# Kernel tuning notes

Hardware: AMD Instinct MI355X
Metric: run time of the kernel (lower is better)

## Reference

```python
import math
import jax, jax.numpy as jnp
import numpy as np

N = 50000          # nodes
E = 800000         # edges
IN_DIM = 128
HID = 128
OUT_DIM = 64
LAYER_NUM = 8      # -> LAYER_NUM - 2 = 6 GCN2Conv layers
NUM_CONVS = LAYER_NUM - 2
ALPHA = 0.1
THETA = 0.5
# PyG GCN2Conv: beta = log(theta / layer + 1); here every conv was built with layer = layer_num + 1
BETA = math.log(THETA / (LAYER_NUM + 1) + 1.0)


def setup_inputs() -> dict:
    key = jax.random.key(0)
    ks = jax.random.split(key, 10)
    x = jax.random.normal(ks[0], (N, IN_DIM), dtype=jnp.float32)
    edge_src = jax.random.randint(ks[1], (E,), 0, N, dtype=jnp.int32)
    edge_dst = jax.random.randint(ks[2], (E,), 0, N, dtype=jnp.int32)
    edge_weight = jax.random.uniform(ks[3], (E,), dtype=jnp.float32)
    s0 = 1.0 / math.sqrt(IN_DIM)
    s1 = 1.0 / math.sqrt(HID)
    W0 = jax.random.uniform(ks[4], (IN_DIM, HID), dtype=jnp.float32, minval=-s0, maxval=s0)
    b0 = jnp.zeros((HID,), dtype=jnp.float32)
    W1 = jax.random.uniform(ks[5], (HID, OUT_DIM), dtype=jnp.float32, minval=-s1, maxval=s1)
    b1 = jnp.zeros((OUT_DIM,), dtype=jnp.float32)
    conv_ws = jax.random.uniform(ks[6], (NUM_CONVS, HID, HID), dtype=jnp.float32, minval=-s1, maxval=s1)
    return {"x": x, "edge_src": edge_src, "edge_dst": edge_dst, "edge_weight": edge_weight,
            "W0": W0, "b0": b0, "W1": W1, "b1": b1, "conv_ws": conv_ws}


def reference(x, edge_src, edge_dst, edge_weight, W0, b0, W1, b1, conv_ws):
    # linear[0] + relu (dropout=0.0 -> identity)
    h = jnp.maximum(x @ W0 + b0, 0.0)          # [N, HID]
    x0 = h
    for i in range(NUM_CONVS):
        # weighted neighbor sum: out[i] = sum_{(j->i)} w_ji * h[j]
        msgs = h[edge_src] * edge_weight[:, None]               # [E, HID]
        agg = jax.ops.segment_sum(msgs, edge_dst, num_segments=N)
        # GCN2Conv (shared_weights=True): z = (1-alpha)*Ah + alpha*x0; out = (1-beta)*z + beta*(z W)
        z = agg * (1.0 - ALPHA) + ALPHA * x0
        h = z * (1.0 - BETA) + BETA * (z @ conv_ws[i])
        h = jnp.maximum(h, 0.0)
    return h @ W1 + b1                          # [N, OUT_DIM]
```

## Files before the change

### kernel.cpp

```cpp
#include <hip/hip_runtime.h>
#include <cstdint>
#include <cstddef>


#define NN 50000
#define EE 800000

constexpr float ALPHA   = 0.1f;
constexpr float BETA_C  = 0.05406722127027574f;

constexpr int NB = (NN + 255) / 256;
constexpr int HB = (EE + 255) / 256;
constexpr int PREP_TOT = 128 * 128 + 6 * 128 * 128 + 64 * 128;
constexpr int PB = (PREP_TOT + 255) / 256;
constexpr int SLICE = NN / 8;
constexpr int NCH = (NN + 31) / 32;

typedef unsigned short u16;
typedef unsigned int   u32;
typedef __attribute__((ext_vector_type(8))) short short8;
typedef __attribute__((ext_vector_type(4))) float f32x4;

__device__ __forceinline__ float bf2f(u16 u) {
    union { float f; u32 i; } c; c.i = ((u32)u) << 16; return c.f;
}
__device__ __forceinline__ u16 f2bf(float f) {
    union { float f; u32 i; } c; c.f = f;
    u32 r = c.i + 0x7fffu + ((c.i >> 16) & 1u);
    return (u16)(r >> 16);
}

__global__ void k_hist_prep(const int* __restrict__ edst, int* __restrict__ deg,
                            const float* __restrict__ W0, const float* __restrict__ cw,
                            const float* __restrict__ W1, u16* __restrict__ w0t,
                            u16* __restrict__ wft, u16* __restrict__ w1t, int E) {
    int b = blockIdx.x;
    if (b < HB) {
        int i = b * 256 + threadIdx.x;
        if (i < E) atomicAdd(&deg[edst[i]], 1);
    } else {
        int i = (b - HB) * 256 + threadIdx.x;
        if (i < 16384) {
            int n = i >> 7, k = i & 127;
            w0t[i] = f2bf(W0[k * 128 + n]);
        } else if (i < 16384 + 6 * 16384) {
            int r = i - 16384;
            int l = r >> 14; int t = r & 16383;
            int n = t >> 7, k = t & 127;
            float v = BETA_C * cw[l * 16384 + k * 128 + n]
                      + ((k == n) ? (1.f - BETA_C) : 0.f);
            wft[r] = f2bf(v);
        } else if (i < PREP_TOT) {
            int r = i - (16384 + 6 * 16384);
            int n = r >> 7, k = r & 127;
            w1t[r] = f2bf(W1[k * 64 + n]);
        }
    }
}

__global__ __launch_bounds__(256) void k_scan_lb(const int* __restrict__ deg,
                                                 int* __restrict__ bsum,
                                                 int* __restrict__ offs,
                                                 int* __restrict__ cur) {
    __shared__ int sh[256];
    __shared__ int sw[4];
    const int c = blockIdx.x, tid = threadIdx.x;
    const int i = c * 256 + tid;
    int v = (i < NN) ? deg[i] : 0;
    sh[tid] = v;
    __syncthreads();
#pragma unroll
    for (int o = 1; o < 256; o <<= 1) {
        int u = (tid >= o) ? sh[tid - o] : 0;
        __syncthreads();
        sh[tid] += u;
        __syncthreads();
    }
    if (tid == 255) atomicExch(&bsum[c], sh[255] + 1);
    int part = 0;
    for (int t = tid; t < c; t += 256) {
        int b;
        do { b = atomicAdd(&bsum[t], 0); } while (b == 0);
        part += b - 1;
    }
#pragma unroll
    for (int o = 32; o > 0; o >>= 1) part += __shfl_down(part, o);
    if ((tid & 63) == 0) sw[tid >> 6] = part;
    __syncthreads();
    const int base = sw[0] + sw[1] + sw[2] + sw[3];
    const int ex = base + sh[tid] - v;
    if (i < NN) {
        offs[i] = ex;
        cur[i]  = ex;
        if (i == NN - 1) offs[NN] = ex + v;
    }
}

__global__ void k_bucket_x(const int* __restrict__ src, const int* __restrict__ dst,
                           const float* __restrict__ w, int* __restrict__ cur,
                           u32* __restrict__ ep, int E) {
    const int slice = blockIdx.x & 7;
    const int i = (blockIdx.x >> 3) * 256 + threadIdx.x;
    if (i >= E) return;
    const int d = dst[i];
    const int lo = slice * SLICE;
    if (d >= lo && d < lo + SLICE) {
        int pos = atomicAdd(&cur[d], 1);
        ep[pos] = ((u32)f2bf(w[i]) << 16) | (u32)src[i];
    }
}

__global__ __launch_bounds__(256) void k_agg_z(const int* __restrict__ offs,
                                               const u32* __restrict__ ep,
                                               const u16* __restrict__ hs,
                                               const u16* __restrict__ x0s,
                                               u16* __restrict__ zs) {
    const int lane = threadIdx.x & 63;
    const int wave = threadIdx.x >> 6;
    const int g  = lane >> 3;
    const int f2 = lane & 7;
    const int s  = blockIdx.y;
    const int n  = blockIdx.x * 32 + wave * 8 + g;
    const int nc = n < NN ? n : NN - 1;
    const uint2* table = (const uint2*)(hs + (size_t)s * NN * 32);

    const int beg = offs[nc], end = offs[nc + 1];
    float a0 = 0.f, a1 = 0.f, a2 = 0.f, a3 = 0.f;
    int e = beg;
    for (; e + 7 < end; e += 8) {
        u32 r[8]; uint2 v[8];
#pragma unroll
        for (int j = 0; j < 8; ++j) r[j] = ep[e + j];
#pragma unroll
        for (int j = 0; j < 8; ++j)
            v[j] = table[(size_t)(r[j] & 0xffffu) * 8 + f2];
#pragma unroll
        for (int j = 0; j < 8; ++j) {
            float w = bf2f((u16)(r[j] >> 16));
            a0 += w * bf2f((u16)v[j].x);  a1 += w * bf2f((u16)(v[j].x >> 16));
            a2 += w * bf2f((u16)v[j].y);  a3 += w * bf2f((u16)(v[j].y >> 16));
        }
    }
    for (; e < end; ++e) {
        u32 r = ep[e];
        uint2 v = table[(size_t)(r & 0xffffu) * 8 + f2];
        float w = bf2f((u16)(r >> 16));
        a0 += w * bf2f((u16)v.x);  a1 += w * bf2f((u16)(v.x >> 16));
        a2 += w * bf2f((u16)v.y);  a3 += w * bf2f((u16)(v.y >> 16));
    }
    if (n < NN) {
        const size_t idx = (size_t)s * NN * 8 + (size_t)n * 8 + f2;
        uint2 xv = ((const uint2*)x0s)[idx];
        float z0 = (1.f - ALPHA) * a0 + ALPHA * bf2f((u16)xv.x);
        float z1 = (1.f - ALPHA) * a1 + ALPHA * bf2f((u16)(xv.x >> 16));
        float z2 = (1.f - ALPHA) * a2 + ALPHA * bf2f((u16)xv.y);
        float z3 = (1.f - ALPHA) * a3 + ALPHA * bf2f((u16)(xv.y >> 16));
        uint2 o;
        o.x = (u32)f2bf(z0) | ((u32)f2bf(z1) << 16);
        o.y = (u32)f2bf(z2) | ((u32)f2bf(z3) << 16);
        ((uint2*)zs)[idx] = o;
    }
}

template <int MODE>
__global__ __launch_bounds__(256) void k_gemm_mfma(const void* __restrict__ Av,
                                                   const u16* __restrict__ Wt,
                                                   const float* __restrict__ bias,
                                                   void* __restrict__ Cv, int M) {
    constexpr int NT = (MODE == 2) ? 4 : 8;
    const int lane = threadIdx.x & 63;
    const int wave = threadIdx.x >> 6;
    const int q = lane >> 4;
    const int m16 = lane & 15;
    const int node = blockIdx.x * 64 + wave * 16 + m16;
    const int nload = node < M ? node : M - 1;

    short8 zf[4];
    if (MODE == 0) {
        const float* xp = (const float*)Av + (size_t)nload * 128 + q * 8;
#pragma unroll
        for (int s = 0; s < 4; ++s) {
            float4 u0 = *(const float4*)(xp + s * 32);
            float4 u1 = *(const float4*)(xp + s * 32 + 4);
            short8 z;
            z[0] = (short)f2bf(u0.x); z[1] = (short)f2bf(u0.y);
            z[2] = (short)f2bf(u0.z); z[3] = (short)f2bf(u0.w);
            z[4] = (short)f2bf(u1.x); z[5] = (short)f2bf(u1.y);
            z[6] = (short)f2bf(u1.z); z[7] = (short)f2bf(u1.w);
            zf[s] = z;
        }
    } else {
        const u16* ap = (const u16*)Av;
#pragma unroll
        for (int s = 0; s < 4; ++s)
            zf[s] = *(const short8*)(ap + (size_t)s * NN * 32 + (size_t)nload * 32 + q * 8);
    }

    f32x4 acc[NT];
#pragma unroll
    for (int c = 0; c < NT; ++c) {
        f32x4 a = {0.f, 0.f, 0.f, 0.f};
        const u16* wp = Wt + (size_t)(c * 16 + m16) * 128 + q * 8;
#pragma unroll
        for (int s = 0; s < 4; ++s) {
            short8 wf = *(const short8*)(wp + s * 32);
            a = __builtin_amdgcn_mfma_f32_16x16x32_bf16(wf, zf[s], a, 0, 0, 0);
        }
        acc[c] = a;
    }

    if (node < M) {
#pragma unroll
        for (int c = 0; c < NT; ++c) {
            const int f0 = c * 16 + q * 4;
            if (MODE == 2) {
                float4 bv = *(const float4*)(bias + f0);
                float4 o;
                o.x = acc[c][0] + bv.x; o.y = acc[c][1] + bv.y;
                o.z = acc[c][2] + bv.z; o.w = acc[c][3] + bv.w;
                *(float4*)((float*)Cv + (size_t)node * 64 + f0) = o;
            } else {
                float v0 = acc[c][0], v1 = acc[c][1], v2 = acc[c][2], v3 = acc[c][3];
                if (MODE == 0) {
                    float4 bv = *(const float4*)(bias + f0);
                    v0 += bv.x; v1 += bv.y; v2 += bv.z; v3 += bv.w;
                }
                v0 = v0 > 0.f ? v0 : 0.f;
                v1 = v1 > 0.f ? v1 : 0.f;
                v2 = v2 > 0.f ? v2 : 0.f;
                v3 = v3 > 0.f ? v3 : 0.f;
                ushort4 o;
                o.x = f2bf(v0); o.y = f2bf(v1); o.z = f2bf(v2); o.w = f2bf(v3);
                *(ushort4*)((u16*)Cv + (size_t)(f0 >> 5) * NN * 32
                            + (size_t)node * 32 + (f0 & 31)) = o;
            }
        }
    }
}


extern "C" void kernel_launch(void* const* d_in, const int* in_sizes, int n_in,
                              void* d_out, int out_size, void* d_ws, size_t ws_size,
                              hipStream_t stream) {
    const float* x    = (const float*)d_in[0];
    const int*   esrc = (const int*)d_in[1];
    const int*   edst = (const int*)d_in[2];
    const float* ew   = (const float*)d_in[3];
    const float* W0   = (const float*)d_in[4];
    const float* b0   = (const float*)d_in[5];
    const float* W1   = (const float*)d_in[6];
    const float* b1   = (const float*)d_in[7];
    const float* cw   = (const float*)d_in[8];
    float* out = (float*)d_out;

    const int N = NN, E = EE;

    u32*  ep4   = (u32*)d_ws;
    u16*  x0s   = (u16*)(ep4 + E);
    u16*  hb1   = x0s + (size_t)4 * N * 32;
    u16*  hb2   = hb1 + (size_t)4 * N * 32;
    u16*  zsb   = hb2 + (size_t)4 * N * 32;
    u16*  w0t   = zsb + (size_t)4 * N * 32;
    u16*  wft   = w0t + 128 * 128;
    u16*  w1t   = wft + 6 * 128 * 128;
    int*  deg   = (int*)(w1t + 64 * 128);
    int*  bsum  = deg  + N;
    int*  offs  = bsum + NB;
    int*  cur   = offs + N + 1;

    hipMemsetAsync(deg, 0, (size_t)(N + NB) * sizeof(int), stream);
    k_hist_prep<<<HB + PB, 256, 0, stream>>>(edst, deg, W0, cw, W1, w0t, wft, w1t, E);
    k_scan_lb<<<NB, 256, 0, stream>>>(deg, bsum, offs, cur);
    k_bucket_x<<<HB * 8, 256, 0, stream>>>(esrc, edst, ew, cur, ep4, E);

    const int gx = (N + 63) / 64;
    const dim3 ga(NCH, 4);

    k_gemm_mfma<0><<<gx, 256, 0, stream>>>(x, w0t, b0, x0s, N);

    const u16* hin = x0s;
    u16* houts[6] = {hb1, hb2, hb1, hb2, hb1, hb2};
    for (int i = 0; i < 6; ++i) {
        k_agg_z<<<ga, 256, 0, stream>>>(offs, ep4, hin, x0s, zsb);
        k_gemm_mfma<1><<<gx, 256, 0, stream>>>(zsb, wft + (size_t)i * 16384,
                                               nullptr, houts[i], N);
        hin = houts[i];
    }

    k_gemm_mfma<2><<<gx, 256, 0, stream>>>(hb2, w1t, b1, out, N);
}
```

Measured before the change: 552.4 us.

## Widen aggregation gathers to 16B per lane and fuse last conv with output GEMM

The aggregation kernel now gives each lane 8 features with uint4 gathers, so 4 lanes cover a 32-feature slice and 16 nodes fit per wave instead of 8. This halves the number of gather instructions and doubles the nodes handled per block. The final conv GEMM and the output projection are fused into one kernel that stages the relu'd hidden tile in LDS, which removes one launch and one hidden-state round trip through global memory. The cost is higher register use in aggregation, fewer lanes per node to spread per-node work, and an extra LDS pass plus a barrier.

After: 546.0 us. About the same (-1.1%).

```diff
diff --git a/kernel.cpp b/kernel.cpp
--- a/kernel.cpp
+++ b/kernel.cpp
@@ -14,7 +14,7 @@
 constexpr int PREP_TOT = 128 * 128 + 6 * 128 * 128 + 64 * 128;
 constexpr int PB = (PREP_TOT + 255) / 256;
 constexpr int SLICE = NN / 8;
-constexpr int NCH = (NN + 31) / 32;
+constexpr int GA = (NN + 63) / 64;
 
 typedef unsigned short u16;
 typedef unsigned int   u32;
@@ -117,48 +117,59 @@
                                                u16* __restrict__ zs) {
     const int lane = threadIdx.x & 63;
     const int wave = threadIdx.x >> 6;
-    const int g  = lane >> 3;
-    const int f2 = lane & 7;
+    const int g  = lane >> 2;
+    const int f4 = lane & 3;
     const int s  = blockIdx.y;
-    const int n  = blockIdx.x * 32 + wave * 8 + g;
+    const int n  = blockIdx.x * 64 + wave * 16 + g;
     const int nc = n < NN ? n : NN - 1;
-    const uint2* table = (const uint2*)(hs + (size_t)s * NN * 32);
+    const uint4* table = (const uint4*)(hs + (size_t)s * NN * 32);
 
     const int beg = offs[nc], end = offs[nc + 1];
     float a0 = 0.f, a1 = 0.f, a2 = 0.f, a3 = 0.f;
+    float a4 = 0.f, a5 = 0.f, a6 = 0.f, a7 = 0.f;
     int e = beg;
     for (; e + 7 < end; e += 8) {
-        u32 r[8]; uint2 v[8];
+        u32 r[8]; uint4 v[8];
 #pragma unroll
         for (int j = 0; j < 8; ++j) r[j] = ep[e + j];
 #pragma unroll
         for (int j = 0; j < 8; ++j)
-            v[j] = table[(size_t)(r[j] & 0xffffu) * 8 + f2];
+            v[j] = table[(size_t)(r[j] & 0xffffu) * 4 + f4];
 #pragma unroll
         for (int j = 0; j < 8; ++j) {
             float w = bf2f((u16)(r[j] >> 16));
             a0 += w * bf2f((u16)v[j].x);  a1 += w * bf2f((u16)(v[j].x >> 16));
             a2 += w * bf2f((u16)v[j].y);  a3 += w * bf2f((u16)(v[j].y >> 16));
+            a4 += w * bf2f((u16)v[j].z);  a5 += w * bf2f((u16)(v[j].z >> 16));
+            a6 += w * bf2f((u16)v[j].w);  a7 += w * bf2f((u16)(v[j].w >> 16));
         }
     }
     for (; e < end; ++e) {
         u32 r = ep[e];
-        uint2 v = table[(size_t)(r & 0xffffu) * 8 + f2];
+        uint4 v = table[(size_t)(r & 0xffffu) * 4 + f4];
         float w = bf2f((u16)(r >> 16));
         a0 += w * bf2f((u16)v.x);  a1 += w * bf2f((u16)(v.x >> 16));
         a2 += w * bf2f((u16)v.y);  a3 += w * bf2f((u16)(v.y >> 16));
+        a4 += w * bf2f((u16)v.z);  a5 += w * bf2f((u16)(v.z >> 16));
+        a6 += w * bf2f((u16)v.w);  a7 += w * bf2f((u16)(v.w >> 16));
     }
     if (n < NN) {
-        const size_t idx = (size_t)s * NN * 8 + (size_t)n * 8 + f2;
-        uint2 xv = ((const uint2*)x0s)[idx];
+        const size_t idx = (size_t)s * NN * 4 + (size_t)n * 4 + f4;
+        uint4 xv = ((const uint4*)x0s)[idx];
         float z0 = (1.f - ALPHA) * a0 + ALPHA * bf2f((u16)xv.x);
         float z1 = (1.f - ALPHA) * a1 + ALPHA * bf2f((u16)(xv.x >> 16));
         float z2 = (1.f - ALPHA) * a2 + ALPHA * bf2f((u16)xv.y);
         float z3 = (1.f - ALPHA) * a3 + ALPHA * bf2f((u16)(xv.y >> 16));
-        uint2 o;
+        float z4 = (1.f - ALPHA) * a4 + ALPHA * bf2f((u16)xv.z);
+        float z5 = (1.f - ALPHA) * a5 + ALPHA * bf2f((u16)(xv.z >> 16));
+        float z6 = (1.f - ALPHA) * a6 + ALPHA * bf2f((u16)xv.w);
+        float z7 = (1.f - ALPHA) * a7 + ALPHA * bf2f((u16)(xv.w >> 16));
+        uint4 o;
         o.x = (u32)f2bf(z0) | ((u32)f2bf(z1) << 16);
         o.y = (u32)f2bf(z2) | ((u32)f2bf(z3) << 16);
-        ((uint2*)zs)[idx] = o;
+        o.z = (u32)f2bf(z4) | ((u32)f2bf(z5) << 16);
+        o.w = (u32)f2bf(z6) | ((u32)f2bf(z7) << 16);
+        ((uint4*)zs)[idx] = o;
     }
 }
 
@@ -167,7 +178,6 @@
                                                    const u16* __restrict__ Wt,
                                                    const float* __restrict__ bias,
                                                    void* __restrict__ Cv, int M) {
-    constexpr int NT = (MODE == 2) ? 4 : 8;
     const int lane = threadIdx.x & 63;
     const int wave = threadIdx.x >> 6;
     const int q = lane >> 4;
@@ -196,9 +206,9 @@
             zf[s] = *(const short8*)(ap + (size_t)s * NN * 32 + (size_t)nload * 32 + q * 8);
     }
 
-    f32x4 acc[NT];
-#pragma unroll
-    for (int c = 0; c < NT; ++c) {
+    f32x4 acc[8];
+#pragma unroll
+    for (int c = 0; c < 8; ++c) {
         f32x4 a = {0.f, 0.f, 0.f, 0.f};
         const u16* wp = Wt + (size_t)(c * 16 + m16) * 128 + q * 8;
 #pragma unroll
@@ -211,28 +221,93 @@
 
     if (node < M) {
 #pragma unroll
-        for (int c = 0; c < NT; ++c) {
+        for (int c = 0; c < 8; ++c) {
             const int f0 = c * 16 + q * 4;
-            if (MODE == 2) {
+            float v0 = acc[c][0], v1 = acc[c][1], v2 = acc[c][2], v3 = acc[c][3];
+            if (MODE == 0) {
                 float4 bv = *(const float4*)(bias + f0);
-                float4 o;
-                o.x = acc[c][0] + bv.x; o.y = acc[c][1] + bv.y;
-                o.z = acc[c][2] + bv.z; o.w = acc[c][3] + bv.w;
-                *(float4*)((float*)Cv + (size_t)node * 64 + f0) = o;
-            } else {
-                float v0 = acc[c][0], v1 = acc[c][1], v2 = acc[c][2], v3 = acc[c][3];
-                if (MODE == 0) {
-                    float4 bv = *(const float4*)(bias + f0);
-                    v0 += bv.x; v1 += bv.y; v2 += bv.z; v3 += bv.w;
-                }
-                v0 = v0 > 0.f ? v0 : 0.f;
-                v1 = v1 > 0.f ? v1 : 0.f;
-                v2 = v2 > 0.f ? v2 : 0.f;
-                v3 = v3 > 0.f ? v3 : 0.f;
-                ushort4 o;
-                o.x = f2bf(v0); o.y = f2bf(v1); o.z = f2bf(v2); o.w = f2bf(v3);
-                *(ushort4*)((u16*)Cv + (size_t)(f0 >> 5) * NN * 32
-                            + (size_t)node * 32 + (f0 & 31)) = o;
+                v0 += bv.x; v1 += bv.y; v2 += bv.z; v3 += bv.w;
+            }
+            v0 = v0 > 0.f ? v0 : 0.f;
+            v1 = v1 > 0.f ? v1 : 0.f;
+            v2 = v2 > 0.f ? v2 : 0.f;
+            v3 = v3 > 0.f ? v3 : 0.f;
+            ushort4 o;
+            o.x = f2bf(v0); o.y = f2bf(v1); o.z = f2bf(v2); o.w = f2bf(v3);
+            *(ushort4*)((u16*)Cv + (size_t)(f0 >> 5) * NN * 32
+                        + (size_t)node * 32 + (f0 & 31)) = o;
+        }
+    }
+}
+
+__global__ __launch_bounds__(256) void k_gemm_last(const u16* __restrict__ z,
+                                                   const u16* __restrict__ wf5,
+                                                   const u16* __restrict__ w1t,
+                                                   const float* __restrict__ b1,
+                                                   float* __restrict__ out) {
+    __shared__ __align__(16) u16 hl[4][16][136];
+    const int lane = threadIdx.x & 63;
+    const int wave = threadIdx.x >> 6;
+    const int q = lane >> 4;
+    const int m16 = lane & 15;
+    const int node = blockIdx.x * 64 + wave * 16 + m16;
+    const int nload = node < NN ? node : NN - 1;
+
+    short8 zf[4];
+#pragma unroll
+    for (int s = 0; s < 4; ++s)
+        zf[s] = *(const short8*)(z + (size_t)s * NN * 32 + (size_t)nload * 32 + q * 8);
+
+#pragma unroll
+    for (int c = 0; c < 8; ++c) {
+        f32x4 a = {0.f, 0.f, 0.f, 0.f};
+        const u16* wp = wf5 + (size_t)(c * 16 + m16) * 128 + q * 8;
+#pragma unroll
+        for (int s = 0; s < 4; ++s) {
+            short8 wf = *(const short8*)(wp + s * 32);
+            a = __builtin_amdgcn_mfma_f32_16x16x32_bf16(wf, zf[s], a, 0, 0, 0);
+        }
+        float v0 = a[0] > 0.f ? a[0] : 0.f;
+        float v1 = a[1] > 0.f ? a[1] : 0.f;
+        float v2 = a[2] > 0.f ? a[2] : 0.f;
+        float v3 = a[3] > 0.f ? a[3] : 0.f;
+        ushort4 o;
+        o.x = f2bf(v0); o.y = f2bf(v1); o.z = f2bf(v2); o.w = f2bf(v3);
+        *(ushort4*)&hl[wave][m16][c * 16 + q * 4] = o;
+    }
+    __syncthreads();
+
+    short8 hf[4];
+#pragma unroll
+    for (int s = 0; s < 4; ++s)
+        hf[s] = *(const short8*)&hl[wave][m16][s * 32 + q * 8];
+
+    if (node < NN) {
+#pragma unroll
+        for (int c = 0; c < 4; ++c) {
+            f32x4 a = {0.f, 0.f, 0.f, 0.f};
+            const u16* wp = w1t + (size_t)(c * 16 + m16) * 128 + q * 8;
+#pragma unroll
+            for (int s = 0; s < 4; ++s) {
+                short8 wf = *(const short8*)(wp + s * 32);
+                a = __builtin_amdgcn_mfma_f32_16x16x32_bf16(wf, hf[s], a, 0, 0, 0);
+            }
+            const int f0 = c * 16 + q * 4;
+            float4 bv = *(const float4*)(b1 + f0);
+            float4 o;
+            o.x = a[0] + bv.x; o.y = a[1] + bv.y;
+            o.z = a[2] + bv.z; o.w = a[3] + bv.w;
+            *(float4*)(out + (size_t)node * 64 + f0) = o;
+        }
+    } else {
+#pragma unroll
+        for (int c = 0; c < 4; ++c) {
+            f32x4 a = {0.f, 0.f, 0.f, 0.f};
+            const u16* wp = w1t + (size_t)(c * 16 + m16) * 128 + q * 8;
+#pragma unroll
+            for (int s = 0; s < 4; ++s) {
+                short8 wf = *(const short8*)(wp + s * 32);
+                a = __builtin_amdgcn_mfma_f32_16x16x32_bf16(wf, hf[s], a, 0, 0, 0);
             }
         }
     }
@@ -273,19 +348,19 @@
     k_scan_lb<<<NB, 256, 0, stream>>>(deg, bsum, offs, cur);
     k_bucket_x<<<HB * 8, 256, 0, stream>>>(esrc, edst, ew, cur, ep4, E);
 
-    const int gx = (N + 63) / 64;
-    const dim3 ga(NCH, 4);
-
-    k_gemm_mfma<0><<<gx, 256, 0, stream>>>(x, w0t, b0, x0s, N);
+    const dim3 ga(GA, 4);
+
+    k_gemm_mfma<0><<<GA, 256, 0, stream>>>(x, w0t, b0, x0s, N);
 
     const u16* hin = x0s;
-    u16* houts[6] = {hb1, hb2, hb1, hb2, hb1, hb2};
-    for (int i = 0; i < 6; ++i) {
+    u16* houts[5] = {hb1, hb2, hb1, hb2, hb1};
+    for (int i = 0; i < 5; ++i) {
         k_agg_z<<<ga, 256, 0, stream>>>(offs, ep4, hin, x0s, zsb);
-        k_gemm_mfma<1><<<gx, 256, 0, stream>>>(zsb, wft + (size_t)i * 16384,
+        k_gemm_mfma<1><<<GA, 256, 0, stream>>>(zsb, wft + (size_t)i * 16384,
                                                nullptr, houts[i], N);
         hin = houts[i];
     }
 
-    k_gemm_mfma<2><<<gx, 256, 0, stream>>>(hb2, w1t, b1, out, N);
-}
+    k_agg_z<<<ga, 256, 0, stream>>>(offs, ep4, hin, x0s, zsb);
+    k_gemm_last<<<GA, 256, 0, stream>>>(zsb, wft + (size_t)5 * 16384, w1t, b1, out);
+}
```
